# Kernel optimization log

Measured on AMD Instinct MI355X. Metric: run time of the kernel, lower is better.

## Reference

```python
import jax, jax.numpy as jnp
import numpy as np

TYPE_NUM = 4
NUM_INPUTS = 128
BATCH = 4096
NODE_NUM = 256
HID = 16


def _xavier_uniform(key, shape, gain=1.414):
    fan_in, fan_out = shape[-2], shape[-1]
    lim = gain * (6.0 / (fan_in + fan_out)) ** 0.5
    return jax.random.uniform(key, shape, jnp.float32, -lim, lim)


def setup_inputs() -> dict:
    key = jax.random.key(0)
    k0, k1, k2, k3, k4 = jax.random.split(key, 5)
    x = jax.random.normal(k0, (BATCH, NODE_NUM, NUM_INPUTS), jnp.float32)
    a1 = _xavier_uniform(k1, (TYPE_NUM, 2 * NUM_INPUTS, HID))
    a2 = _xavier_uniform(k2, (TYPE_NUM, HID, 1))
    # binary neighbor mask over nodes; ensure at least one neighbor
    adj_mask = jax.random.randint(k3, (NODE_NUM,), 0, 2).astype(jnp.float32).at[0].set(1.0)
    type_index = jax.random.randint(k4, (BATCH,), 0, TYPE_NUM)
    node_index = 0
    return dict(x=x, a1=a1, a2=a2, adj_mask=adj_mask,
                node_index=node_index, type_index=type_index)


def reference(x, a1, a2, adj_mask, node_index, type_index):
    # x: [B, N, F]; a1: [T, 2F, H]; a2: [T, H, 1]; adj_mask: [N]; type_index: [B]
    B, N, Fdim = x.shape
    T = a1.shape[0]
    tgt = jnp.broadcast_to(x[:, node_index, :][:, None, :], (B, N, Fdim))
    concat = jnp.concatenate([tgt, x], axis=-1)            # [B, N, 2F]
    h = jax.nn.leaky_relu(jnp.einsum('bnc,tch->tbnh', concat, a1))   # [T, B, N, H]
    e = jax.nn.leaky_relu(jnp.einsum('tbnh,th->tbn', h, a2[:, :, 0]))  # [T, B, N]
    neg = jnp.asarray(-9e15, e.dtype)
    att = jnp.where(adj_mask > 0, e, neg)                  # mask broadcasts over [T,B,N]
    att = jax.nn.softmax(att, axis=-1) * adj_mask          # [T, B, N]
    onehot = jax.nn.one_hot(type_index, T, dtype=x.dtype)  # [B, T]
    probs = jnp.einsum('tbn,bt->bn', att, onehot)          # [B, N] -> Categorical probs
    return probs
```

## Files before the change

kernel.cpp:

```cpp
#include <hip/hip_runtime.h>
#include <math.h>

#define BATCH 4096
#define NODES 256
#define FDIM  128
#define HID   16

typedef __attribute__((ext_vector_type(8))) short short8;
typedef __attribute__((ext_vector_type(4))) float f32x4;

__device__ __forceinline__ short bf_rn(float x) {
    const unsigned u = __float_as_uint(x);
    return (short)((u + 0x7FFF + ((u >> 16) & 1)) >> 16);
}
__device__ __forceinline__ float bf_back(short s) {
    return __uint_as_float(((unsigned)(unsigned short)s) << 16);
}
__device__ __forceinline__ void split8(float4 v0, float4 v1,
                                       short8& hi, short8& lo) {
    float v[8] = {v0.x, v0.y, v0.z, v0.w, v1.x, v1.y, v1.z, v1.w};
    #pragma unroll
    for (int j = 0; j < 8; ++j) {
        const short h = bf_rn(v[j]);
        hi[j] = h;
        lo[j] = bf_rn(v[j] - bf_back(h));
    }
}

__launch_bounds__(256, 3)
__global__ void mta_kernel(const float* __restrict__ x,
                           const float* __restrict__ a1,
                           const float* __restrict__ a2,
                           const float* __restrict__ adj,
                           const int*  __restrict__ node_index,
                           const int*  __restrict__ type_index,
                           float* __restrict__ out) {
    const int b    = blockIdx.x;
    const int tid  = threadIdx.x;
    const int lane = tid & 63;
    const int w    = tid >> 6;
    const int n    = lane & 15;
    const int g    = lane >> 4;

    __shared__ float es[NODES];
    __shared__ float part[16][17];
    __shared__ float c0s[HID];
    __shared__ float redm[4], reds[4];

    const int t  = __builtin_amdgcn_readfirstlane(type_index[b]);
    const int ni = __builtin_amdgcn_readfirstlane(node_index[0]);

    const float* At  = a1 + (size_t)t * (2 * FDIM * HID);
    const float* Ab  = At + FDIM * HID;
    const float* a2t = a2 + t * HID;
    const float* xb  = x + (size_t)b * NODES * FDIM;

    {
        const float* x0 = xb + (size_t)ni * FDIM;
        const int f2 = tid >> 4;
        const int h  = tid & 15;
        float p = 0.f;
        #pragma unroll
        for (int j = 0; j < 8; ++j) {
            const int f = f2 * 8 + j;
            p = fmaf(x0[f], At[f * HID + h], p);
        }
        part[f2][h] = p;
    }
    __syncthreads();
    if (tid < 16) {
        float s = 0.f;
        #pragma unroll
        for (int gg = 0; gg < 16; ++gg) s += part[gg][tid];
        c0s[tid] = s;
    }
    __syncthreads();

    short8 whi[4];
    #pragma unroll
    for (int kt = 0; kt < 4; ++kt) {
        #pragma unroll
        for (int j = 0; j < 8; ++j)
            whi[kt][j] = bf_rn(Ab[(kt * 32 + g * 8 + j) * HID + n]);
    }

    const int rowbase = w * 64;
    f32x4 acc[4];
    #pragma unroll
    for (int mt = 0; mt < 4; ++mt) acc[mt] = (f32x4){0.f, 0.f, 0.f, 0.f};

    #pragma unroll
    for (int kt = 0; kt < 4; ++kt) {
        #pragma unroll
        for (int mh = 0; mh < 4; mh += 2) {
            float4 ra[2][2];
            #pragma unroll
            for (int i = 0; i < 2; ++i) {
                const float* p = xb
                    + (size_t)(rowbase + (mh + i) * 16 + n) * FDIM
                    + kt * 32 + g * 8;
                ra[i][0] = *(const float4*)p;
                ra[i][1] = *(const float4*)(p + 4);
            }
            #pragma unroll
            for (int i = 0; i < 2; ++i) {
                short8 ahi, alo;
                split8(ra[i][0], ra[i][1], ahi, alo);
                acc[mh + i] = __builtin_amdgcn_mfma_f32_16x16x32_bf16(
                    ahi, whi[kt], acc[mh + i], 0, 0, 0);
                acc[mh + i] = __builtin_amdgcn_mfma_f32_16x16x32_bf16(
                    alo, whi[kt], acc[mh + i], 0, 0, 0);
            }
        }
    }

    const float c0h = c0s[n];
    const float a2h = a2t[n];
    #pragma unroll
    for (int mt = 0; mt < 4; ++mt) {
        #pragma unroll
        for (int r = 0; r < 4; ++r) {
            float v = acc[mt][r] + c0h;
            v = (v > 0.f) ? v : 0.01f * v;
            float s = v * a2h;
            s += __shfl_xor(s, 1);
            s += __shfl_xor(s, 2);
            s += __shfl_xor(s, 4);
            s += __shfl_xor(s, 8);
            float e = (s > 0.f) ? s : 0.01f * s;
            if (n == 0) es[rowbase + mt * 16 + g * 4 + r] = e;
        }
    }
    __syncthreads();

    const float ee  = es[tid];
    const float m   = adj[tid];
    float       val = (m > 0.f) ? ee : -INFINITY;

    float mx = val;
    #pragma unroll
    for (int off = 32; off; off >>= 1) mx = fmaxf(mx, __shfl_xor(mx, off));
    const int wid = tid >> 6;
    if ((tid & 63) == 0) redm[wid] = mx;
    __syncthreads();
    mx = fmaxf(fmaxf(redm[0], redm[1]), fmaxf(redm[2], redm[3]));

    float pr = (m > 0.f) ? __expf(ee - mx) : 0.f;
    float s = pr;
    #pragma unroll
    for (int off = 32; off; off >>= 1) s += __shfl_xor(s, off);
    if ((tid & 63) == 0) reds[wid] = s;
    __syncthreads();
    const float Z = reds[0] + reds[1] + reds[2] + reds[3];

    out[(size_t)b * NODES + tid] = pr / Z;
}

extern "C" void kernel_launch(void* const* d_in, const int* in_sizes, int n_in,
                              void* d_out, int out_size, void* d_ws, size_t ws_size,
                              hipStream_t stream) {
    const float* x   = (const float*)d_in[0];
    const float* a1  = (const float*)d_in[1];
    const float* a2  = (const float*)d_in[2];
    const float* adj = (const float*)d_in[3];
    const int*   ni  = (const int*)d_in[4];
    const int*   ti  = (const int*)d_in[5];
    float* out = (float*)d_out;

    mta_kernel<<<BATCH, NODES, 0, stream>>>(x, a1, a2, adj, ni, ti, out);
}
```

Before: 105.4 us.

## Assign one wavefront per batch item to remove block-level barriers

Changes the work split so each 64-lane wavefront handles a whole batch element (256 nodes), with four batch elements per block, instead of one block per batch element. The target-node projection and both softmax reductions now use wave shuffles rather than shared memory and __syncthreads. Each wave loops over 16 row tiles, issuing its loads before its MFMAs, and writes the output with float4 stores. The trade-off is less parallelism inside each batch item, since each wave runs its 16 tiles in sequence with a non-unrolled loop, and the occupancy hint is removed.

```diff
diff --git a/kernel.cpp b/kernel.cpp
--- a/kernel.cpp
+++ b/kernel.cpp
@@ -27,7 +27,7 @@
     }
 }
 
-__launch_bounds__(256, 3)
+__launch_bounds__(256)
 __global__ void mta_kernel(const float* __restrict__ x,
                            const float* __restrict__ a1,
                            const float* __restrict__ a2,
@@ -35,17 +35,14 @@
                            const int*  __restrict__ node_index,
                            const int*  __restrict__ type_index,
                            float* __restrict__ out) {
-    const int b    = blockIdx.x;
     const int tid  = threadIdx.x;
     const int lane = tid & 63;
     const int w    = tid >> 6;
+    const int b    = blockIdx.x * 4 + w;
     const int n    = lane & 15;
     const int g    = lane >> 4;
 
-    __shared__ float es[NODES];
-    __shared__ float part[16][17];
-    __shared__ float c0s[HID];
-    __shared__ float redm[4], reds[4];
+    __shared__ float es[4][NODES];
 
     const int t  = __builtin_amdgcn_readfirstlane(type_index[b]);
     const int ni = __builtin_amdgcn_readfirstlane(node_index[0]);
@@ -55,105 +52,88 @@
     const float* a2t = a2 + t * HID;
     const float* xb  = x + (size_t)b * NODES * FDIM;
 
+    float c0 = 0.f;
     {
-        const float* x0 = xb + (size_t)ni * FDIM;
-        const int f2 = tid >> 4;
-        const int h  = tid & 15;
-        float p = 0.f;
+        const float* x0  = xb + (size_t)ni * FDIM + g * 32;
+        const float* Atg = At + (g * 32) * HID + n;
         #pragma unroll
-        for (int j = 0; j < 8; ++j) {
-            const int f = f2 * 8 + j;
-            p = fmaf(x0[f], At[f * HID + h], p);
+        for (int j4 = 0; j4 < 8; ++j4) {
+            const float4 xv = *(const float4*)(x0 + j4 * 4);
+            c0 = fmaf(xv.x, Atg[(j4 * 4 + 0) * HID], c0);
+            c0 = fmaf(xv.y, Atg[(j4 * 4 + 1) * HID], c0);
+            c0 = fmaf(xv.z, Atg[(j4 * 4 + 2) * HID], c0);
+            c0 = fmaf(xv.w, Atg[(j4 * 4 + 3) * HID], c0);
         }
-        part[f2][h] = p;
+        c0 += __shfl_xor(c0, 16);
+        c0 += __shfl_xor(c0, 32);
     }
-    __syncthreads();
-    if (tid < 16) {
-        float s = 0.f;
-        #pragma unroll
-        for (int gg = 0; gg < 16; ++gg) s += part[gg][tid];
-        c0s[tid] = s;
-    }
-    __syncthreads();
 
-    short8 whi[4];
+    short8 wfrag[4];
     #pragma unroll
     for (int kt = 0; kt < 4; ++kt) {
         #pragma unroll
         for (int j = 0; j < 8; ++j)
-            whi[kt][j] = bf_rn(Ab[(kt * 32 + g * 8 + j) * HID + n]);
+            wfrag[kt][j] = bf_rn(Ab[(kt * 32 + g * 8 + j) * HID + n]);
     }
+    const float a2h = a2t[n];
 
-    const int rowbase = w * 64;
-    f32x4 acc[4];
-    #pragma unroll
-    for (int mt = 0; mt < 4; ++mt) acc[mt] = (f32x4){0.f, 0.f, 0.f, 0.f};
-
-    #pragma unroll
-    for (int kt = 0; kt < 4; ++kt) {
+    float* esw = es[w];
+    #pragma unroll 1
+    for (int mt = 0; mt < 16; ++mt) {
+        float4 ra[4][2];
         #pragma unroll
-        for (int mh = 0; mh < 4; mh += 2) {
-            float4 ra[2][2];
-            #pragma unroll
-            for (int i = 0; i < 2; ++i) {
-                const float* p = xb
-                    + (size_t)(rowbase + (mh + i) * 16 + n) * FDIM
-                    + kt * 32 + g * 8;
-                ra[i][0] = *(const float4*)p;
-                ra[i][1] = *(const float4*)(p + 4);
-            }
-            #pragma unroll
-            for (int i = 0; i < 2; ++i) {
-                short8 ahi, alo;
-                split8(ra[i][0], ra[i][1], ahi, alo);
-                acc[mh + i] = __builtin_amdgcn_mfma_f32_16x16x32_bf16(
-                    ahi, whi[kt], acc[mh + i], 0, 0, 0);
-                acc[mh + i] = __builtin_amdgcn_mfma_f32_16x16x32_bf16(
-                    alo, whi[kt], acc[mh + i], 0, 0, 0);
-            }
+        for (int kt = 0; kt < 4; ++kt) {
+            const float* p = xb + (size_t)(mt * 16 + n) * FDIM
+                           + kt * 32 + g * 8;
+            ra[kt][0] = *(const float4*)p;
+            ra[kt][1] = *(const float4*)(p + 4);
         }
-    }
-
-    const float c0h = c0s[n];
-    const float a2h = a2t[n];
-    #pragma unroll
-    for (int mt = 0; mt < 4; ++mt) {
+        f32x4 acc = (f32x4){0.f, 0.f, 0.f, 0.f};
+        #pragma unroll
+        for (int kt = 0; kt < 4; ++kt) {
+            short8 ahi, alo;
+            split8(ra[kt][0], ra[kt][1], ahi, alo);
+            acc = __builtin_amdgcn_mfma_f32_16x16x32_bf16(ahi, wfrag[kt], acc, 0, 0, 0);
+            acc = __builtin_amdgcn_mfma_f32_16x16x32_bf16(alo, wfrag[kt], acc, 0, 0, 0);
+        }
         #pragma unroll
         for (int r = 0; r < 4; ++r) {
-            float v = acc[mt][r] + c0h;
+            float v = acc[r] + c0;
             v = (v > 0.f) ? v : 0.01f * v;
             float s = v * a2h;
             s += __shfl_xor(s, 1);
             s += __shfl_xor(s, 2);
             s += __shfl_xor(s, 4);
             s += __shfl_xor(s, 8);
-            float e = (s > 0.f) ? s : 0.01f * s;
-            if (n == 0) es[rowbase + mt * 16 + g * 4 + r] = e;
+            const float e = (s > 0.f) ? s : 0.01f * s;
+            if (n == 0) esw[mt * 16 + g * 4 + r] = e;
         }
     }
-    __syncthreads();
 
-    const float ee  = es[tid];
-    const float m   = adj[tid];
-    float       val = (m > 0.f) ? ee : -INFINITY;
+    const float4 ev = *(const float4*)&esw[lane * 4];
+    const float4 mv = *(const float4*)&adj[lane * 4];
+    const float NEG = -INFINITY;
+    float e0 = (mv.x > 0.f) ? ev.x : NEG;
+    float e1 = (mv.y > 0.f) ? ev.y : NEG;
+    float e2 = (mv.z > 0.f) ? ev.z : NEG;
+    float e3 = (mv.w > 0.f) ? ev.w : NEG;
 
-    float mx = val;
+    float mx = fmaxf(fmaxf(e0, e1), fmaxf(e2, e3));
     #pragma unroll
     for (int off = 32; off; off >>= 1) mx = fmaxf(mx, __shfl_xor(mx, off));
-    const int wid = tid >> 6;
-    if ((tid & 63) == 0) redm[wid] = mx;
-    __syncthreads();
-    mx = fmaxf(fmaxf(redm[0], redm[1]), fmaxf(redm[2], redm[3]));
 
-    float pr = (m > 0.f) ? __expf(ee - mx) : 0.f;
-    float s = pr;
+    const float p0 = (mv.x > 0.f) ? __expf(e0 - mx) : 0.f;
+    const float p1 = (mv.y > 0.f) ? __expf(e1 - mx) : 0.f;
+    const float p2 = (mv.z > 0.f) ? __expf(e2 - mx) : 0.f;
+    const float p3 = (mv.w > 0.f) ? __expf(e3 - mx) : 0.f;
+
+    float s = (p0 + p1) + (p2 + p3);
     #pragma unroll
     for (int off = 32; off; off >>= 1) s += __shfl_xor(s, off);
-    if ((tid & 63) == 0) reds[wid] = s;
-    __syncthreads();
-    const float Z = reds[0] + reds[1] + reds[2] + reds[3];
+    const float rz = 1.f / s;
 
-    out[(size_t)b * NODES + tid] = pr / Z;
+    float4 ov = {p0 * rz, p1 * rz, p2 * rz, p3 * rz};
+    *(float4*)&out[(size_t)b * NODES + lane * 4] = ov;
 }
 
 extern "C" void kernel_launch(void* const* d_in, const int* in_sizes, int n_in,
@@ -167,5 +147,5 @@
     const int*   ti  = (const int*)d_in[5];
     float* out = (float*)d_out;
 
-    mta_kernel<<<BATCH, NODES, 0, stream>>>(x, a1, a2, adj, ni, ti, out);
+    mta_kernel<<<BATCH / 4, 256, 0, stream>>>(x, a1, a2, adj, ni, ti, out);
 }
```

New measurement: 109.0 us. 3.4% more time.
